# Optimization experiments

Measured on AMD Instinct MI355X. Metric: run time of the kernel, lower is better.

## Reference

```python
import jax, jax.numpy as jnp
import numpy as np
import math

B, N, C = 8, 4096, 768
H = 12
DH = C // H
M = 256
LN_EPS = 1e-5


def setup_inputs() -> dict:
    key = jax.random.key(0)
    ks = jax.random.split(key, 7)
    x = jax.random.normal(ks[0], (B, N, C), dtype=jnp.float32)
    # torch Linear weight [out,in]; store transposed for y = x @ W
    W_qkv = jax.random.normal(ks[1], (C, 3 * C), dtype=jnp.float32) * (1.0 / math.sqrt(C))
    W_proj = jax.random.normal(ks[2], (C, C), dtype=jnp.float32) * (1.0 / math.sqrt(C))
    b_proj = jnp.zeros((C,), dtype=jnp.float32)
    gamma = jnp.ones((C,), dtype=jnp.float32)
    beta = jnp.zeros((C,), dtype=jnp.float32)
    random_features = jax.random.normal(ks[3], (M, DH), dtype=jnp.float32) / math.sqrt(DH)
    return {"x": x, "W_qkv": W_qkv, "W_proj": W_proj, "b_proj": b_proj,
            "gamma": gamma, "beta": beta, "random_features": random_features}


def _phi(t, random_features):
    # t: [B, H, N, DH] -> [B, H, N, M]; phi(x) = exp(w·x - ||x||^2/2) / sqrt(M)
    norm_sq = 0.5 * jnp.sum(t * t, axis=-1, keepdims=True)
    proj = jnp.einsum('bhnd,md->bhnm', t, random_features)
    return jnp.exp(proj - norm_sq) * (1.0 / math.sqrt(M))


def reference(x, W_qkv, W_proj, b_proj, gamma, beta, random_features):
    b, n, c = x.shape
    qkv = (x @ W_qkv).reshape(b, n, 3, H, DH)
    qkv = jnp.transpose(qkv, (2, 0, 3, 1, 4))  # [3, B, H, N, DH]
    q, k, v = qkv[0], qkv[1], qkv[2]

    q_p = _phi(q, random_features)  # [B,H,N,M]
    k_p = _phi(k, random_features)  # [B,H,N,M]

    kv = jnp.einsum('bhnm,bhnd->bhmd', k_p, v)       # [B,H,M,DH]
    out = jnp.einsum('bhnm,bhmd->bhnd', q_p, kv)     # [B,H,N,DH]

    k_sum = jnp.sum(k_p, axis=2)                      # [B,H,M]
    normalizer = jnp.einsum('bhnm,bhm->bhn', q_p, k_sum)[..., None]
    out = out / (normalizer + 1e-6)

    x_attn = jnp.transpose(out, (0, 2, 1, 3)).reshape(b, n, c)
    x_attn = x_attn @ W_proj + b_proj
    # dropout is identity in eval / p=0

    y = x + x_attn
    mu = jnp.mean(y, axis=-1, keepdims=True)
    var = jnp.mean(jnp.square(y - mu), axis=-1, keepdims=True)
    return (y - mu) * jax.lax.rsqrt(var + LN_EPS) * gamma + beta
```

## Files before the change

kernel.cpp:

```cpp
#include <hip/hip_runtime.h>
#include <hip/hip_fp16.h>


#define LOG2E 1.44269504088896340736f

typedef _Float16 half8 __attribute__((ext_vector_type(8)));
typedef _Float16 half4_t __attribute__((ext_vector_type(4)));
typedef _Float16 half2_t __attribute__((ext_vector_type(2)));
typedef float f32x4 __attribute__((ext_vector_type(4)));

#if __has_builtin(__builtin_amdgcn_fdot2)
#define FDOT2(a, b, c) __builtin_amdgcn_fdot2((a), (b), (c), false)
#else
#define FDOT2(a, b, c) \
  ((float)(a)[0] * (float)(b)[0] + ((float)(a)[1] * (float)(b)[1] + (c)))
#endif

static __device__ __forceinline__ half2_t pk2(float a, float b) {
#if __has_builtin(__builtin_amdgcn_cvt_pkrtz)
  return __builtin_bit_cast(half2_t, __builtin_amdgcn_cvt_pkrtz(a, b));
#else
  half2_t r; r[0] = (_Float16)a; r[1] = (_Float16)b; return r;
#endif
}


__global__ __launch_bounds__(256) void cast_f32_f16(const float* __restrict__ in,
                                                    _Float16* __restrict__ out, long n) {
  long i = ((long)blockIdx.x * 256 + threadIdx.x) * 4;
  if (i + 3 < n) {
    float4 v = *(const float4*)(in + i);
    half4_t h;
    h[0] = (_Float16)v.x; h[1] = (_Float16)v.y; h[2] = (_Float16)v.z; h[3] = (_Float16)v.w;
    *(half4_t*)(out + i) = h;
  } else {
    for (long j = i; j < n && j < i + 4; ++j) out[j] = (_Float16)in[j];
  }
}

__global__ __launch_bounds__(256) void cast_transpose(const float* __restrict__ in,
                                                      _Float16* __restrict__ out,
                                                      int K, int Nt) {
  long i = (long)blockIdx.x * 256 + threadIdx.x;
  if (i >= (long)K * Nt) return;
  int n = (int)(i % Nt);
  int k = (int)(i / Nt);
  out[(long)n * K + k] = (_Float16)in[i];
}


__device__ __forceinline__ void glds16(const _Float16* g, _Float16* s) {
  __builtin_amdgcn_global_load_lds(
      (const __attribute__((address_space(1))) void*)g,
      (__attribute__((address_space(3))) unsigned int*)s,
      16, 0, 0);
}

template <int EPI>
__global__ __launch_bounds__(256)
void gemm_f16(const _Float16* __restrict__ A, const _Float16* __restrict__ BT,
              float* __restrict__ Co, int Mr, int Ntot, int K,
              const float* __restrict__ bias, const float* __restrict__ resid,
              _Float16* __restrict__ qh, _Float16* __restrict__ kh,
              _Float16* __restrict__ vT) {
  __shared__ __align__(16) _Float16 As[128 * 32];
  __shared__ __align__(16) _Float16 Bs[128 * 32];
  const int tid = threadIdx.x;
  const int w = tid >> 6;
  const int l = tid & 63;
  const int lr = l & 15;
  const int kg = l >> 4;
  const int m0 = blockIdx.y * 128;
  const int n0 = blockIdx.x * 128;
  const int wm = (w >> 1) * 64;
  const int wn = (w & 1) * 64;

  const _Float16* gA = A + (long)(m0 + w * 32 + (l >> 2)) * K + (l & 3) * 8;
  const _Float16* gB = BT + (long)(n0 + w * 32 + (l >> 2)) * K + (l & 3) * 8;
  _Float16* sA = As + (w * 32) * 32;
  _Float16* sB = Bs + (w * 32) * 32;

  f32x4 acc[4][4];
#pragma unroll
  for (int t = 0; t < 4; ++t)
#pragma unroll
    for (int u = 0; u < 4; ++u) acc[t][u] = (f32x4){0.f, 0.f, 0.f, 0.f};

  const int nK = K >> 5;
  for (int kc = 0; kc < nK; ++kc) {
    __syncthreads();
    glds16(gA, sA);
    glds16(gA + 16 * K, sA + 16 * 32);
    glds16(gB, sB);
    glds16(gB + 16 * K, sB + 16 * 32);
    gA += 32; gB += 32;
    __syncthreads();

    half8 af[4], bf[4];
#pragma unroll
    for (int t = 0; t < 4; ++t)
      af[t] = *(const half8*)(As + (wm + t * 16 + lr) * 32 + kg * 8);
#pragma unroll
    for (int u = 0; u < 4; ++u)
      bf[u] = *(const half8*)(Bs + (wn + u * 16 + lr) * 32 + kg * 8);
#pragma unroll
    for (int t = 0; t < 4; ++t)
#pragma unroll
      for (int u = 0; u < 4; ++u)
        acc[t][u] = __builtin_amdgcn_mfma_f32_16x16x32_f16(af[t], bf[u], acc[t][u], 0, 0, 0);
  }

#pragma unroll
  for (int t = 0; t < 4; ++t)
#pragma unroll
    for (int u = 0; u < 4; ++u) {
      const int row = m0 + wm + t * 16 + kg * 4;
      const int col = n0 + wn + u * 16 + lr;
      if (EPI == 1) {
#pragma unroll
        for (int r = 0; r < 4; ++r) {
          long idx = (long)(row + r) * Ntot + col;
          Co[idx] = acc[t][u][r] + bias[col] + resid[idx];
        }
      } else {
        const int which = (col >= 1536) ? 2 : ((col >= 768) ? 1 : 0);
        const int c2 = col - which * 768;
        const int h = c2 >> 6, d = c2 & 63;
        const int b_ = row >> 12, n_ = row & 4095;
        if (which == 2) {
          half4_t p4;
#pragma unroll
          for (int r = 0; r < 4; ++r) p4[r] = (_Float16)acc[t][u][r];
          *(half4_t*)(vT + ((long)(b_ * 12 + h) * 64 + d) * 4096 + n_) = p4;
        } else {
          _Float16* dst = (which == 0) ? qh : kh;
#pragma unroll
          for (int r = 0; r < 4; ++r)
            dst[((long)(b_ * 12 + h) * 4096 + n_ + r) * 64 + d] = (_Float16)acc[t][u][r];
        }
      }
    }
}


__global__ __launch_bounds__(256)
void nsq_kernel(const _Float16* __restrict__ qh, const _Float16* __restrict__ kh,
                float* __restrict__ nsqLq, float* __restrict__ nsqLk) {
  long idx = (long)blockIdx.x * 256 + threadIdx.x;
  const long base = idx * 64;
  float sq = 0.f, sk = 0.f;
#pragma unroll
  for (int d = 0; d < 64; d += 8) {
    half8 a = *(const half8*)(qh + base + d);
    half8 c = *(const half8*)(kh + base + d);
#pragma unroll
    for (int j = 0; j < 8; ++j) {
      float fa = (float)a[j], fc = (float)c[j];
      sq += fa * fa;
      sk += fc * fc;
    }
  }
  nsqLq[idx] = 0.5f * sq * LOG2E + 4.0f;
  nsqLk[idx] = 0.5f * sk * LOG2E + 4.0f;
}


__global__ __launch_bounds__(256)
void kv_fused(const _Float16* __restrict__ kh, const _Float16* __restrict__ vT,
              const _Float16* __restrict__ rfh, const float* __restrict__ nsqLk,
              _Float16* __restrict__ kvpart, float* __restrict__ kspart) {
  __shared__ __align__(16) _Float16 Ka[64 * 32], Kb[64 * 32];
  __shared__ __align__(16) _Float16 Va[64 * 32], Vb[64 * 32];
  __shared__ __align__(16) _Float16 P[256 * 72];
  const int chunk = blockIdx.x, bh = blockIdx.y;
  const int tid = threadIdx.x, w = tid >> 6, l = tid & 63;
  const int lr = l & 15, kg = l >> 4;
  const long khbase = (long)bh * 4096 * 64;
  const long vtbase = (long)bh * 64 * 4096;
  const half2_t ONES = {(_Float16)1.f, (_Float16)1.f};

  half8 rf[4][2];
#pragma unroll
  for (int u = 0; u < 4; ++u)
#pragma unroll
    for (int ks = 0; ks < 2; ++ks)
      rf[u][ks] = *(const half8*)(rfh + (w * 64 + u * 16 + lr) * 64 + ks * 32 + kg * 8);

  f32x4 kvacc[4][4];
#pragma unroll
  for (int mt = 0; mt < 4; ++mt)
#pragma unroll
    for (int dt = 0; dt < 4; ++dt) kvacc[mt][dt] = (f32x4){0.f, 0.f, 0.f, 0.f};
  float ksacc[4] = {0.f, 0.f, 0.f, 0.f};

  for (int t8 = 0; t8 < 4; ++t8) {
    const int nt = chunk * 256 + t8 * 64;
    __syncthreads();
    if (w == 0) {
#pragma unroll
      for (int j = 0; j < 4; ++j)
        glds16(kh + khbase + (long)(nt + j * 16 + (l >> 2)) * 64 + (l & 3) * 8, Ka + j * 512);
    } else if (w == 1) {
#pragma unroll
      for (int j = 0; j < 4; ++j)
        glds16(kh + khbase + (long)(nt + j * 16 + (l >> 2)) * 64 + 32 + (l & 3) * 8, Kb + j * 512);
    } else if (w == 2) {
#pragma unroll
      for (int j = 0; j < 4; ++j)
        glds16(vT + vtbase + (long)(j * 16 + (l >> 2)) * 4096 + nt + (l & 3) * 8, Va + j * 512);
    } else {
#pragma unroll
      for (int j = 0; j < 4; ++j)
        glds16(vT + vtbase + (long)(j * 16 + (l >> 2)) * 4096 + nt + 32 + (l & 3) * 8, Vb + j * 512);
    }
    __syncthreads();

    half8 af[4][2];
#pragma unroll
    for (int tt = 0; tt < 4; ++tt) {
      af[tt][0] = *(const half8*)(Ka + (tt * 16 + lr) * 32 + kg * 8);
      af[tt][1] = *(const half8*)(Kb + (tt * 16 + lr) * 32 + kg * 8);
    }
    f32x4 sacc[4][4];
#pragma unroll
    for (int tt = 0; tt < 4; ++tt)
#pragma unroll
      for (int u = 0; u < 4; ++u) sacc[tt][u] = (f32x4){0.f, 0.f, 0.f, 0.f};
#pragma unroll
    for (int ks = 0; ks < 2; ++ks)
#pragma unroll
      for (int tt = 0; tt < 4; ++tt)
#pragma unroll
        for (int u = 0; u < 4; ++u)
          sacc[tt][u] = __builtin_amdgcn_mfma_f32_16x16x32_f16(af[tt][ks], rf[u][ks],
                                                               sacc[tt][u], 0, 0, 0);
    float4 nsq4[4];
#pragma unroll
    for (int tt = 0; tt < 4; ++tt)
      nsq4[tt] = *(const float4*)(nsqLk + (long)bh * 4096 + nt + tt * 16 + kg * 4);
#pragma unroll
    for (int tt = 0; tt < 4; ++tt)
#pragma unroll
      for (int u = 0; u < 4; ++u) {
        float e0 = exp2f(sacc[tt][u][0] * LOG2E - nsq4[tt].x);
        float e1 = exp2f(sacc[tt][u][1] * LOG2E - nsq4[tt].y);
        float e2 = exp2f(sacc[tt][u][2] * LOG2E - nsq4[tt].z);
        float e3 = exp2f(sacc[tt][u][3] * LOG2E - nsq4[tt].w);
        half2_t h01 = pk2(e0, e1), h23 = pk2(e2, e3);
        half4_t p4; p4[0] = h01[0]; p4[1] = h01[1]; p4[2] = h23[0]; p4[3] = h23[1];
        *(half4_t*)(P + (w * 64 + u * 16 + lr) * 72 + tt * 16 + kg * 4) = p4;
      }

#pragma unroll
    for (int ks = 0; ks < 2; ++ks) {
      half8 pa[4], bv[4];
#pragma unroll
      for (int mt = 0; mt < 4; ++mt)
        pa[mt] = *(const half8*)(P + (w * 64 + mt * 16 + lr) * 72 + ks * 32 + kg * 8);
#pragma unroll
      for (int dt = 0; dt < 4; ++dt)
        bv[dt] = *(const half8*)((ks == 0 ? Va : Vb) + (dt * 16 + lr) * 32 + kg * 8);
#pragma unroll
      for (int mt = 0; mt < 4; ++mt)
#pragma unroll
        for (int dt = 0; dt < 4; ++dt)
          kvacc[mt][dt] = __builtin_amdgcn_mfma_f32_16x16x32_f16(pa[mt], bv[dt],
                                                                 kvacc[mt][dt], 0, 0, 0);
#pragma unroll
      for (int mt = 0; mt < 4; ++mt) {
        const half2_t* pp = (const half2_t*)&pa[mt];
#pragma unroll
        for (int p = 0; p < 4; ++p) ksacc[mt] = FDOT2(pp[p], ONES, ksacc[mt]);
      }
    }
  }

#pragma unroll
  for (int mt = 0; mt < 4; ++mt) {
    float v = ksacc[mt];
    v += __shfl_xor(v, 16);
    v += __shfl_xor(v, 32);
    if (l < 16) kspart[((bh * 16 + chunk) << 8) + w * 64 + mt * 16 + l] = v;
  }
#pragma unroll
  for (int mt = 0; mt < 4; ++mt)
#pragma unroll
    for (int dt = 0; dt < 4; ++dt)
#pragma unroll
      for (int r = 0; r < 4; ++r)
        kvpart[(((long)(bh * 16 + chunk) * 256) + w * 64 + mt * 16 + kg * 4 + r) * 64 +
               dt * 16 + lr] = (_Float16)kvacc[mt][dt][r];
}

__global__ __launch_bounds__(256)
void reduce_kv(const _Float16* __restrict__ part, _Float16* __restrict__ kvT) {
  long i = (long)blockIdx.x * 256 + threadIdx.x;
  const int bh = (int)(i >> 14);
  const int rem = (int)(i & 16383);
  const int m = rem >> 6, d = rem & 63;
  float s = 0.f;
#pragma unroll
  for (int c = 0; c < 16; ++c)
    s += (float)part[(((long)bh * 16 + c) * 256 + m) * 64 + d];
  kvT[(long)bh * 16384 + d * 256 + m] = (_Float16)s;
}

__global__ __launch_bounds__(256)
void reduce_ks(const float* __restrict__ part, _Float16* __restrict__ ksumh) {
  int i = blockIdx.x * 256 + threadIdx.x;
  int bh = i >> 8, m = i & 255;
  float s = 0.f;
#pragma unroll
  for (int c = 0; c < 16; ++c) s += part[((bh * 16 + c) << 8) + m];
  ksumh[i] = (_Float16)s;
}


__global__ __launch_bounds__(256)
void attn_fused(const _Float16* __restrict__ qh, const _Float16* __restrict__ rfh,
                const float* __restrict__ nsqLq, const _Float16* __restrict__ kvT,
                const _Float16* __restrict__ ksumh, _Float16* __restrict__ attn) {
  __shared__ __align__(16) _Float16 Qa[64 * 32], Qb[64 * 32];
  __shared__ __align__(16) _Float16 KV[64 * 264];
  __shared__ __align__(16) _Float16 KS[256];
  __shared__ __align__(16) _Float16 P[64 * 264];
  __shared__ __align__(16) float NS[64];
  const int chunk = blockIdx.x, bh = blockIdx.y;
  const int b = bh / 12, h = bh % 12;
  const int tid = threadIdx.x, w = tid >> 6, l = tid & 63;
  const int lr = l & 15, kg = l >> 4;

  {
    const int d = tid >> 2, mb = (tid & 3) * 64;
#pragma unroll
    for (int j = 0; j < 8; ++j)
      *(half8*)(KV + d * 264 + mb + j * 8) =
          *(const half8*)(kvT + (long)bh * 16384 + d * 256 + mb + j * 8);
    if (tid < 32) *(half8*)(KS + tid * 8) = *(const half8*)(ksumh + bh * 256 + tid * 8);
  }

  half8 rf[4][2];
#pragma unroll
  for (int mt = 0; mt < 4; ++mt)
#pragma unroll
    for (int ks = 0; ks < 2; ++ks)
      rf[mt][ks] = *(const half8*)(rfh + (w * 64 + mt * 16 + lr) * 64 + ks * 32 + kg * 8);

  for (int t8 = 0; t8 < 4; ++t8) {
    const int nt = chunk * 256 + t8 * 64;
    __syncthreads();
    if (w == 0) {
#pragma unroll
      for (int j = 0; j < 4; ++j)
        glds16(qh + ((long)bh * 4096 + nt + j * 16 + (l >> 2)) * 64 + (l & 3) * 8, Qa + j * 512);
    } else if (w == 1) {
#pragma unroll
      for (int j = 0; j < 4; ++j)
        glds16(qh + ((long)bh * 4096 + nt + j * 16 + (l >> 2)) * 64 + 32 + (l & 3) * 8, Qb + j * 512);
    }
    __syncthreads();

    half8 bq[4][2];
#pragma unroll
    for (int tt = 0; tt < 4; ++tt) {
      bq[tt][0] = *(const half8*)(Qa + (tt * 16 + lr) * 32 + kg * 8);
      bq[tt][1] = *(const half8*)(Qb + (tt * 16 + lr) * 32 + kg * 8);
    }
    f32x4 sacc[4][4];
#pragma unroll
    for (int mt = 0; mt < 4; ++mt)
#pragma unroll
      for (int tt = 0; tt < 4; ++tt) sacc[mt][tt] = (f32x4){0.f, 0.f, 0.f, 0.f};
#pragma unroll
    for (int ks = 0; ks < 2; ++ks)
#pragma unroll
      for (int mt = 0; mt < 4; ++mt)
#pragma unroll
        for (int tt = 0; tt < 4; ++tt)
          sacc[mt][tt] = __builtin_amdgcn_mfma_f32_16x16x32_f16(rf[mt][ks], bq[tt][ks],
                                                                sacc[mt][tt], 0, 0, 0);
    float nsqv[4];
#pragma unroll
    for (int tt = 0; tt < 4; ++tt)
      nsqv[tt] = nsqLq[(long)bh * 4096 + nt + tt * 16 + lr];
#pragma unroll
    for (int mt = 0; mt < 4; ++mt)
#pragma unroll
      for (int tt = 0; tt < 4; ++tt) {
        float e0 = exp2f(sacc[mt][tt][0] * LOG2E - nsqv[tt]);
        float e1 = exp2f(sacc[mt][tt][1] * LOG2E - nsqv[tt]);
        float e2 = exp2f(sacc[mt][tt][2] * LOG2E - nsqv[tt]);
        float e3 = exp2f(sacc[mt][tt][3] * LOG2E - nsqv[tt]);
        half2_t h01 = pk2(e0, e1), h23 = pk2(e2, e3);
        half4_t p4; p4[0] = h01[0]; p4[1] = h01[1]; p4[2] = h23[0]; p4[3] = h23[1];
        *(half4_t*)(P + (tt * 16 + lr) * 264 + w * 64 + mt * 16 + kg * 4) = p4;
      }
    __syncthreads();

    f32x4 oacc[4];
#pragma unroll
    for (int u = 0; u < 4; ++u) oacc[u] = (f32x4){0.f, 0.f, 0.f, 0.f};
    float nacc = 0.f;
#pragma unroll
    for (int ks = 0; ks < 8; ++ks) {
      half8 ap = *(const half8*)(P + (w * 16 + lr) * 264 + ks * 32 + kg * 8);
      half8 kv8 = *(const half8*)(KS + ks * 32 + kg * 8);
      const half2_t* a2 = (const half2_t*)&ap;
      const half2_t* k2 = (const half2_t*)&kv8;
#pragma unroll
      for (int p = 0; p < 4; ++p) nacc = FDOT2(a2[p], k2[p], nacc);
#pragma unroll
      for (int u = 0; u < 4; ++u) {
        half8 bkv = *(const half8*)(KV + (u * 16 + lr) * 264 + ks * 32 + kg * 8);
        oacc[u] = __builtin_amdgcn_mfma_f32_16x16x32_f16(ap, bkv, oacc[u], 0, 0, 0);
      }
    }
    nacc += __shfl_xor(nacc, 16);
    nacc += __shfl_xor(nacc, 32);
    if (l < 16) NS[w * 16 + l] = nacc;
    f32x4 n4 = *(const f32x4*)(NS + w * 16 + kg * 4);
    float inv[4];
#pragma unroll
    for (int r = 0; r < 4; ++r) inv[r] = 1.f / (n4[r] + 1e-6f);
#pragma unroll
    for (int u = 0; u < 4; ++u)
#pragma unroll
      for (int r = 0; r < 4; ++r)
        attn[((long)b * 4096 + nt + w * 16 + kg * 4 + r) * 768 + h * 64 + u * 16 + lr] =
            (_Float16)(oacc[u][r] * inv[r]);
  }
}


__global__ __launch_bounds__(256)
void ln_kernel(const float* __restrict__ y, const float* __restrict__ gamma,
               const float* __restrict__ beta, float* __restrict__ outp) {
  const int wv = threadIdx.x >> 6, l = threadIdx.x & 63;
  const long row = (long)blockIdx.x * 4 + wv;
  const float* yr = y + row * 768;
  float v[12];
  float s = 0.f;
#pragma unroll
  for (int j = 0; j < 12; ++j) { v[j] = yr[l + j * 64]; s += v[j]; }
#pragma unroll
  for (int off = 32; off; off >>= 1) s += __shfl_xor(s, off);
  const float mu = s * (1.f / 768.f);
  float vs = 0.f;
#pragma unroll
  for (int j = 0; j < 12; ++j) { float d = v[j] - mu; vs += d * d; }
#pragma unroll
  for (int off = 32; off; off >>= 1) vs += __shfl_xor(vs, off);
  const float rstd = rsqrtf(vs * (1.f / 768.f) + 1e-5f);
  float* orp = outp + row * 768;
#pragma unroll
  for (int j = 0; j < 12; ++j)
    orp[l + j * 64] = (v[j] - mu) * rstd * gamma[l + j * 64] + beta[l + j * 64];
}


extern "C" void kernel_launch(void* const* d_in, const int* in_sizes, int n_in,
                              void* d_out, int out_size, void* d_ws, size_t ws_size,
                              hipStream_t stream) {
  const float* x = (const float*)d_in[0];
  const float* Wqkv = (const float*)d_in[1];
  const float* Wproj = (const float*)d_in[2];
  const float* bproj = (const float*)d_in[3];
  const float* gamma = (const float*)d_in[4];
  const float* beta = (const float*)d_in[5];
  const float* rfm = (const float*)d_in[6];

  char* ws = (char*)d_ws;
  size_t off = 0;
  auto alloc = [&](size_t bytes) -> void* {
    void* p = ws + off;
    off += (bytes + 255) & ~(size_t)255;
    return p;
  };
  char* regionA = (char*)alloc(50331648ULL);
  _Float16* x_h = (_Float16*)regionA;
  _Float16* kvpart = (_Float16*)regionA;
  _Float16* attn = (_Float16*)regionA;

  _Float16* wqkvT = (_Float16*)alloc(1769472ULL * 2);
  _Float16* wprojT = (_Float16*)alloc(589824ULL * 2);
  _Float16* rfh = (_Float16*)alloc(16384ULL * 2);
  _Float16* qh = (_Float16*)alloc(25165824ULL * 2);
  _Float16* kh = (_Float16*)alloc(25165824ULL * 2);
  _Float16* vT = (_Float16*)alloc(25165824ULL * 2);
  float* nsqLq = (float*)alloc(393216ULL * 4);
  float* nsqLk = (float*)alloc(393216ULL * 4);
  float* kspart = (float*)alloc(96ULL * 16 * 256 * 4);
  _Float16* kvT = (_Float16*)alloc(96ULL * 16384 * 2);
  _Float16* ksumh = (_Float16*)alloc(96ULL * 256 * 2);

  float* y = (float*)d_out;

  cast_f32_f16<<<24576, 256, 0, stream>>>(x, x_h, 25165824L);
  cast_transpose<<<6912, 256, 0, stream>>>(Wqkv, wqkvT, 768, 2304);
  cast_transpose<<<2304, 256, 0, stream>>>(Wproj, wprojT, 768, 768);
  cast_f32_f16<<<16, 256, 0, stream>>>(rfm, rfh, 16384L);
  gemm_f16<2><<<dim3(18, 256), 256, 0, stream>>>(x_h, wqkvT, nullptr, 32768, 2304, 768,
                                                 nullptr, nullptr, qh, kh, vT);
  nsq_kernel<<<1536, 256, 0, stream>>>(qh, kh, nsqLq, nsqLk);
  kv_fused<<<dim3(16, 96), 256, 0, stream>>>(kh, vT, rfh, nsqLk, kvpart, kspart);
  reduce_kv<<<6144, 256, 0, stream>>>(kvpart, kvT);
  reduce_ks<<<96, 256, 0, stream>>>(kspart, ksumh);
  attn_fused<<<dim3(16, 96), 256, 0, stream>>>(qh, rfh, nsqLq, kvT, ksumh, attn);
  gemm_f16<1><<<dim3(6, 256), 256, 0, stream>>>(attn, wprojT, y, 32768, 768, 768,
                                                bproj, x, nullptr, nullptr, nullptr);
  ln_kernel<<<8192, 256, 0, stream>>>(y, gamma, beta, y);
}
```

Baseline: 659.5 us.

## Fuse prep casts, fold norm computation into QKV GEMM, halve KV partials

```diff
diff --git a/kernel.cpp b/kernel.cpp
--- a/kernel.cpp
+++ b/kernel.cpp
@@ -24,31 +24,6 @@
 #endif
 }
 
-
-__global__ __launch_bounds__(256) void cast_f32_f16(const float* __restrict__ in,
-                                                    _Float16* __restrict__ out, long n) {
-  long i = ((long)blockIdx.x * 256 + threadIdx.x) * 4;
-  if (i + 3 < n) {
-    float4 v = *(const float4*)(in + i);
-    half4_t h;
-    h[0] = (_Float16)v.x; h[1] = (_Float16)v.y; h[2] = (_Float16)v.z; h[3] = (_Float16)v.w;
-    *(half4_t*)(out + i) = h;
-  } else {
-    for (long j = i; j < n && j < i + 4; ++j) out[j] = (_Float16)in[j];
-  }
-}
-
-__global__ __launch_bounds__(256) void cast_transpose(const float* __restrict__ in,
-                                                      _Float16* __restrict__ out,
-                                                      int K, int Nt) {
-  long i = (long)blockIdx.x * 256 + threadIdx.x;
-  if (i >= (long)K * Nt) return;
-  int n = (int)(i % Nt);
-  int k = (int)(i / Nt);
-  out[(long)n * K + k] = (_Float16)in[i];
-}
-
-
 __device__ __forceinline__ void glds16(const _Float16* g, _Float16* s) {
   __builtin_amdgcn_global_load_lds(
       (const __attribute__((address_space(1))) void*)g,
@@ -56,27 +31,147 @@
       16, 0, 0);
 }
 
-template <int EPI>
-__global__ __launch_bounds__(256)
-void gemm_f16(const _Float16* __restrict__ A, const _Float16* __restrict__ BT,
-              float* __restrict__ Co, int Mr, int Ntot, int K,
-              const float* __restrict__ bias, const float* __restrict__ resid,
+
+__global__ __launch_bounds__(256)
+void prep(const float* __restrict__ x, const float* __restrict__ Wqkv,
+          const float* __restrict__ Wproj, const float* __restrict__ rfm,
+          _Float16* __restrict__ x_h, _Float16* __restrict__ wqkvT,
+          _Float16* __restrict__ wprojT, _Float16* __restrict__ rfh) {
+  const long bid = blockIdx.x;
+  if (bid < 24576) {
+    long i = (bid * 256 + threadIdx.x) * 4;
+    float4 v = *(const float4*)(x + i);
+    half4_t h;
+    h[0] = (_Float16)v.x; h[1] = (_Float16)v.y; h[2] = (_Float16)v.z; h[3] = (_Float16)v.w;
+    *(half4_t*)(x_h + i) = h;
+    return;
+  }
+  long idx = (bid - 24576) * 256 + threadIdx.x;
+  if (idx < 1769472) {
+    int k = (int)(idx / 2304), n = (int)(idx % 2304);
+    wqkvT[(long)n * 768 + k] = (_Float16)Wqkv[idx];
+  } else if ((idx -= 1769472) < 589824) {
+    int k = (int)(idx / 768), n = (int)(idx % 768);
+    wprojT[(long)n * 768 + k] = (_Float16)Wproj[idx];
+  } else if ((idx -= 589824) < 16384) {
+    rfh[idx] = (_Float16)rfm[idx];
+  }
+}
+
+
+__global__ __launch_bounds__(256)
+void gemm_qkv(const _Float16* __restrict__ W, const _Float16* __restrict__ X,
               _Float16* __restrict__ qh, _Float16* __restrict__ kh,
-              _Float16* __restrict__ vT) {
+              _Float16* __restrict__ vT,
+              float* __restrict__ nsqLq, float* __restrict__ nsqLk) {
   __shared__ __align__(16) _Float16 As[128 * 32];
   __shared__ __align__(16) _Float16 Bs[128 * 32];
   const int tid = threadIdx.x;
-  const int w = tid >> 6;
-  const int l = tid & 63;
-  const int lr = l & 15;
-  const int kg = l >> 4;
+  const int w = tid >> 6, l = tid & 63;
+  const int lr = l & 15, kg = l >> 4;
+  const int m0 = blockIdx.x * 128;
+  const int n0 = blockIdx.y * 128;
+  const int wm = (w >> 1) * 64, wn = (w & 1) * 64;
+
+  const _Float16* gA = W + (long)(m0 + w * 32 + (l >> 2)) * 768 + (l & 3) * 8;
+  const _Float16* gB = X + (long)(n0 + w * 32 + (l >> 2)) * 768 + (l & 3) * 8;
+  _Float16* sA = As + (w * 32) * 32;
+  _Float16* sB = Bs + (w * 32) * 32;
+
+  f32x4 acc[4][4];
+#pragma unroll
+  for (int t = 0; t < 4; ++t)
+#pragma unroll
+    for (int u = 0; u < 4; ++u) acc[t][u] = (f32x4){0.f, 0.f, 0.f, 0.f};
+
+  for (int kc = 0; kc < 24; ++kc) {
+    __syncthreads();
+    glds16(gA, sA);
+    glds16(gA + 16 * 768, sA + 16 * 32);
+    glds16(gB, sB);
+    glds16(gB + 16 * 768, sB + 16 * 32);
+    gA += 32; gB += 32;
+    __syncthreads();
+
+    half8 af[4], bf[4];
+#pragma unroll
+    for (int t = 0; t < 4; ++t)
+      af[t] = *(const half8*)(As + (wm + t * 16 + lr) * 32 + kg * 8);
+#pragma unroll
+    for (int u = 0; u < 4; ++u)
+      bf[u] = *(const half8*)(Bs + (wn + u * 16 + lr) * 32 + kg * 8);
+#pragma unroll
+    for (int t = 0; t < 4; ++t)
+#pragma unroll
+      for (int u = 0; u < 4; ++u)
+        acc[t][u] = __builtin_amdgcn_mfma_f32_16x16x32_f16(af[t], bf[u], acc[t][u], 0, 0, 0);
+  }
+
+  const int which = (m0 >= 1536) ? 2 : ((m0 >= 768) ? 1 : 0);
+  const int base = (m0 - which * 768) + wm;
+  const int h = base >> 6;
+
+  if (which < 2) {
+    _Float16* dst = (which == 0) ? qh : kh;
+    float* nd = (which == 0) ? nsqLq : nsqLk;
+    float ns[4] = {0.f, 0.f, 0.f, 0.f};
+#pragma unroll
+    for (int u = 0; u < 4; ++u) {
+      const int tok = n0 + wn + u * 16 + lr;
+      const int b_ = tok >> 12, n_ = tok & 4095;
+      const long rowbase = ((long)(b_ * 12 + h) * 4096 + n_) * 64;
+#pragma unroll
+      for (int t = 0; t < 4; ++t) {
+        half2_t h01 = pk2(acc[t][u][0], acc[t][u][1]);
+        half2_t h23 = pk2(acc[t][u][2], acc[t][u][3]);
+        half4_t p4; p4[0] = h01[0]; p4[1] = h01[1]; p4[2] = h23[0]; p4[3] = h23[1];
+        *(half4_t*)(dst + rowbase + t * 16 + kg * 4) = p4;
+#pragma unroll
+        for (int r = 0; r < 4; ++r) { float f = (float)p4[r]; ns[u] += f * f; }
+      }
+    }
+#pragma unroll
+    for (int u = 0; u < 4; ++u) {
+      float s = ns[u];
+      s += __shfl_xor(s, 16);
+      s += __shfl_xor(s, 32);
+      if (kg == 0) {
+        const int tok = n0 + wn + u * 16 + lr;
+        const int b_ = tok >> 12, n_ = tok & 4095;
+        nd[(long)(b_ * 12 + h) * 4096 + n_] = 0.5f * s * LOG2E + 4.0f;
+      }
+    }
+  } else {
+#pragma unroll
+    for (int u = 0; u < 4; ++u) {
+      const int tok = n0 + wn + u * 16 + lr;
+      const int b_ = tok >> 12, n_ = tok & 4095;
+      const long hb = (long)(b_ * 12 + h) * 64;
+#pragma unroll
+      for (int t = 0; t < 4; ++t)
+#pragma unroll
+        for (int r = 0; r < 4; ++r)
+          vT[(hb + t * 16 + kg * 4 + r) * 4096 + n_] = (_Float16)acc[t][u][r];
+    }
+  }
+}
+
+
+__global__ __launch_bounds__(256)
+void gemm_proj(const _Float16* __restrict__ A, const _Float16* __restrict__ BT,
+               float* __restrict__ Co, const float* __restrict__ bias,
+               const float* __restrict__ resid) {
+  __shared__ __align__(16) _Float16 As[128 * 32];
+  __shared__ __align__(16) _Float16 Bs[128 * 32];
+  const int tid = threadIdx.x;
+  const int w = tid >> 6, l = tid & 63;
+  const int lr = l & 15, kg = l >> 4;
   const int m0 = blockIdx.y * 128;
   const int n0 = blockIdx.x * 128;
-  const int wm = (w >> 1) * 64;
-  const int wn = (w & 1) * 64;
-
-  const _Float16* gA = A + (long)(m0 + w * 32 + (l >> 2)) * K + (l & 3) * 8;
-  const _Float16* gB = BT + (long)(n0 + w * 32 + (l >> 2)) * K + (l & 3) * 8;
+  const int wm = (w >> 1) * 64, wn = (w & 1) * 64;
+
+  const _Float16* gA = A + (long)(m0 + w * 32 + (l >> 2)) * 768 + (l & 3) * 8;
+  const _Float16* gB = BT + (long)(n0 + w * 32 + (l >> 2)) * 768 + (l & 3) * 8;
   _Float16* sA = As + (w * 32) * 32;
   _Float16* sB = Bs + (w * 32) * 32;
 
@@ -86,13 +181,12 @@
 #pragma unroll
     for (int u = 0; u < 4; ++u) acc[t][u] = (f32x4){0.f, 0.f, 0.f, 0.f};
 
-  const int nK = K >> 5;
-  for (int kc = 0; kc < nK; ++kc) {
+  for (int kc = 0; kc < 24; ++kc) {
     __syncthreads();
     glds16(gA, sA);
-    glds16(gA + 16 * K, sA + 16 * 32);
+    glds16(gA + 16 * 768, sA + 16 * 32);
     glds16(gB, sB);
-    glds16(gB + 16 * K, sB + 16 * 32);
+    glds16(gB + 16 * 768, sB + 16 * 32);
     gA += 32; gB += 32;
     __syncthreads();
 
@@ -111,57 +205,19 @@
   }
 
 #pragma unroll
-  for (int t = 0; t < 4; ++t)
-#pragma unroll
-    for (int u = 0; u < 4; ++u) {
+  for (int u = 0; u < 4; ++u) {
+    const int col = n0 + wn + u * 16 + lr;
+    const float bv = bias[col];
+#pragma unroll
+    for (int t = 0; t < 4; ++t) {
       const int row = m0 + wm + t * 16 + kg * 4;
-      const int col = n0 + wn + u * 16 + lr;
-      if (EPI == 1) {
-#pragma unroll
-        for (int r = 0; r < 4; ++r) {
-          long idx = (long)(row + r) * Ntot + col;
-          Co[idx] = acc[t][u][r] + bias[col] + resid[idx];
-        }
-      } else {
-        const int which = (col >= 1536) ? 2 : ((col >= 768) ? 1 : 0);
-        const int c2 = col - which * 768;
-        const int h = c2 >> 6, d = c2 & 63;
-        const int b_ = row >> 12, n_ = row & 4095;
-        if (which == 2) {
-          half4_t p4;
-#pragma unroll
-          for (int r = 0; r < 4; ++r) p4[r] = (_Float16)acc[t][u][r];
-          *(half4_t*)(vT + ((long)(b_ * 12 + h) * 64 + d) * 4096 + n_) = p4;
-        } else {
-          _Float16* dst = (which == 0) ? qh : kh;
-#pragma unroll
-          for (int r = 0; r < 4; ++r)
-            dst[((long)(b_ * 12 + h) * 4096 + n_ + r) * 64 + d] = (_Float16)acc[t][u][r];
-        }
-      }
-    }
-}
-
-
-__global__ __launch_bounds__(256)
-void nsq_kernel(const _Float16* __restrict__ qh, const _Float16* __restrict__ kh,
-                float* __restrict__ nsqLq, float* __restrict__ nsqLk) {
-  long idx = (long)blockIdx.x * 256 + threadIdx.x;
-  const long base = idx * 64;
-  float sq = 0.f, sk = 0.f;
-#pragma unroll
-  for (int d = 0; d < 64; d += 8) {
-    half8 a = *(const half8*)(qh + base + d);
-    half8 c = *(const half8*)(kh + base + d);
-#pragma unroll
-    for (int j = 0; j < 8; ++j) {
-      float fa = (float)a[j], fc = (float)c[j];
-      sq += fa * fa;
-      sk += fc * fc;
-    }
-  }
-  nsqLq[idx] = 0.5f * sq * LOG2E + 4.0f;
-  nsqLk[idx] = 0.5f * sk * LOG2E + 4.0f;
+#pragma unroll
+      for (int r = 0; r < 4; ++r) {
+        long idx = (long)(row + r) * 768 + col;
+        Co[idx] = acc[t][u][r] + bv + resid[idx];
+      }
+    }
+  }
 }
 
 
@@ -193,8 +249,8 @@
     for (int dt = 0; dt < 4; ++dt) kvacc[mt][dt] = (f32x4){0.f, 0.f, 0.f, 0.f};
   float ksacc[4] = {0.f, 0.f, 0.f, 0.f};
 
-  for (int t8 = 0; t8 < 4; ++t8) {
-    const int nt = chunk * 256 + t8 * 64;
+  for (int t8 = 0; t8 < 8; ++t8) {
+    const int nt = chunk * 512 + t8 * 64;
     __syncthreads();
     if (w == 0) {
 #pragma unroll
@@ -250,7 +306,6 @@
         half4_t p4; p4[0] = h01[0]; p4[1] = h01[1]; p4[2] = h23[0]; p4[3] = h23[1];
         *(half4_t*)(P + (w * 64 + u * 16 + lr) * 72 + tt * 16 + kg * 4) = p4;
       }
-
 #pragma unroll
     for (int ks = 0; ks < 2; ++ks) {
       half8 pa[4], bv[4];
@@ -280,7 +335,7 @@
     float v = ksacc[mt];
     v += __shfl_xor(v, 16);
     v += __shfl_xor(v, 32);
-    if (l < 16) kspart[((bh * 16 + chunk) << 8) + w * 64 + mt * 16 + l] = v;
+    if (l < 16) kspart[((bh * 8 + chunk) << 8) + w * 64 + mt * 16 + l] = v;
   }
 #pragma unroll
   for (int mt = 0; mt < 4; ++mt)
@@ -288,31 +343,32 @@
     for (int dt = 0; dt < 4; ++dt)
 #pragma unroll
       for (int r = 0; r < 4; ++r)
-        kvpart[(((long)(bh * 16 + chunk) * 256) + w * 64 + mt * 16 + kg * 4 + r) * 64 +
+        kvpart[(((long)(bh * 8 + chunk) * 256) + w * 64 + mt * 16 + kg * 4 + r) * 64 +
                dt * 16 + lr] = (_Float16)kvacc[mt][dt][r];
 }
 
-__global__ __launch_bounds__(256)
-void reduce_kv(const _Float16* __restrict__ part, _Float16* __restrict__ kvT) {
-  long i = (long)blockIdx.x * 256 + threadIdx.x;
-  const int bh = (int)(i >> 14);
-  const int rem = (int)(i & 16383);
-  const int m = rem >> 6, d = rem & 63;
-  float s = 0.f;
-#pragma unroll
-  for (int c = 0; c < 16; ++c)
-    s += (float)part[(((long)bh * 16 + c) * 256 + m) * 64 + d];
-  kvT[(long)bh * 16384 + d * 256 + m] = (_Float16)s;
-}
-
-__global__ __launch_bounds__(256)
-void reduce_ks(const float* __restrict__ part, _Float16* __restrict__ ksumh) {
-  int i = blockIdx.x * 256 + threadIdx.x;
-  int bh = i >> 8, m = i & 255;
-  float s = 0.f;
-#pragma unroll
-  for (int c = 0; c < 16; ++c) s += part[((bh * 16 + c) << 8) + m];
-  ksumh[i] = (_Float16)s;
+
+__global__ __launch_bounds__(256)
+void reduce_all(const _Float16* __restrict__ kvpart, const float* __restrict__ kspart,
+                _Float16* __restrict__ kvT, _Float16* __restrict__ ksumh) {
+  if (blockIdx.x < 6144) {
+    long i = (long)blockIdx.x * 256 + threadIdx.x;
+    const int bh = (int)(i >> 14);
+    const int rem = (int)(i & 16383);
+    const int m = rem >> 6, d = rem & 63;
+    float s = 0.f;
+#pragma unroll
+    for (int c = 0; c < 8; ++c)
+      s += (float)kvpart[(((long)bh * 8 + c) * 256 + m) * 64 + d];
+    kvT[(long)bh * 16384 + d * 256 + m] = (_Float16)s;
+  } else {
+    int i = (blockIdx.x - 6144) * 256 + threadIdx.x;
+    int bh = i >> 8, m = i & 255;
+    float s = 0.f;
+#pragma unroll
+    for (int c = 0; c < 8; ++c) s += kspart[((bh * 8 + c) << 8) + m];
+    ksumh[i] = (_Float16)s;
+  }
 }
 
 
@@ -489,24 +545,17 @@
   _Float16* vT = (_Float16*)alloc(25165824ULL * 2);
   float* nsqLq = (float*)alloc(393216ULL * 4);
   float* nsqLk = (float*)alloc(393216ULL * 4);
-  float* kspart = (float*)alloc(96ULL * 16 * 256 * 4);
+  float* kspart = (float*)alloc(96ULL * 8 * 256 * 4);
   _Float16* kvT = (_Float16*)alloc(96ULL * 16384 * 2);
   _Float16* ksumh = (_Float16*)alloc(96ULL * 256 * 2);
 
   float* y = (float*)d_out;
 
-  cast_f32_f16<<<24576, 256, 0, stream>>>(x, x_h, 25165824L);
-  cast_transpose<<<6912, 256, 0, stream>>>(Wqkv, wqkvT, 768, 2304);
-  cast_transpose<<<2304, 256, 0, stream>>>(Wproj, wprojT, 768, 768);
-  cast_f32_f16<<<16, 256, 0, stream>>>(rfm, rfh, 16384L);
-  gemm_f16<2><<<dim3(18, 256), 256, 0, stream>>>(x_h, wqkvT, nullptr, 32768, 2304, 768,
-                                                 nullptr, nullptr, qh, kh, vT);
-  nsq_kernel<<<1536, 256, 0, stream>>>(qh, kh, nsqLq, nsqLk);
-  kv_fused<<<dim3(16, 96), 256, 0, stream>>>(kh, vT, rfh, nsqLk, kvpart, kspart);
-  reduce_kv<<<6144, 256, 0, stream>>>(kvpart, kvT);
-  reduce_ks<<<96, 256, 0, stream>>>(kspart, ksumh);
+  prep<<<33856, 256, 0, stream>>>(x, Wqkv, Wproj, rfm, x_h, wqkvT, wprojT, rfh);
+  gemm_qkv<<<dim3(18, 256), 256, 0, stream>>>(wqkvT, x_h, qh, kh, vT, nsqLq, nsqLk);
+  kv_fused<<<dim3(8, 96), 256, 0, stream>>>(kh, vT, rfh, nsqLk, kvpart, kspart);
+  reduce_all<<<6240, 256, 0, stream>>>(kvpart, kspart, kvT, ksumh);
   attn_fused<<<dim3(16, 96), 256, 0, stream>>>(qh, rfh, nsqLq, kvT, ksumh, attn);
-  gemm_f16<1><<<dim3(6, 256), 256, 0, stream>>>(attn, wprojT, y, 32768, 768, 768,
-                                                bproj, x, nullptr, nullptr, nullptr);
+  gemm_proj<<<dim3(6, 256), 256, 0, stream>>>(attn, wprojT, y, bproj, x);
   ln_kernel<<<8192, 256, 0, stream>>>(y, gamma, beta, y);
 }
```

Result: faster. 621.6 us (-5.7%).
